# Optimization experiments

Measured on AMD Instinct MI355X. Metric: run time of the kernel, lower is better.

## Reference

```python
import jax, jax.numpy as jnp
import numpy as np

EPS_LN = 1e-5

def layer_norm(x, w, b):
    u = x.mean(-1, keepdims=True)
    s = jnp.mean((x - u) ** 2, -1, keepdims=True)
    return w * ((x - u) / jnp.sqrt(s + EPS_LN)) + b

def mlp(x, W, b, lw, lb):
    return jax.nn.relu(layer_norm(x @ W + b, lw, lb))

def mlp_gate(x, W, b, lw, lb):
    return jax.nn.sigmoid(layer_norm(x @ W + b, lw, lb))

def setup_inputs() -> dict:
    N, D = 768, 64
    key = jax.random.key(0)
    ks = jax.random.split(key, 12)
    inp = {
        'corr_index': jax.random.normal(ks[0], (N, N, 2), jnp.float32),
        'nei_index': jax.random.randint(ks[1], (N, N), 0, 2).astype(jnp.int64),
        'nei_num': jax.random.randint(ks[2], (N,), 0, N).astype(jnp.int64),
        'hidden_state': jax.random.normal(ks[3], (N, D), jnp.float32),
        'agent_v': jax.random.normal(ks[4], (N, 2), jnp.float32),
        # relativeLayer: MLP(3, D)
        'rel_w': jax.random.normal(ks[5], (3, D), jnp.float32) * (1.0 / np.sqrt(3)),
        'rel_b': jnp.zeros((D,), jnp.float32),
        'rel_lw': jnp.ones((D,), jnp.float32),
        'rel_lb': jnp.zeros((D,), jnp.float32),
        # ngate: MLP_gate(3D, D)
        'ng_w': jax.random.normal(ks[6], (3 * D, D), jnp.float32) * (1.0 / np.sqrt(3 * D)),
        'ng_b': jnp.zeros((D,), jnp.float32),
        'ng_lw': jnp.ones((D,), jnp.float32),
        'ng_lb': jnp.zeros((D,), jnp.float32),
        # WAr: MLP(3D, 1) -- LayerNorm(1) is identity in the source
        'war_w': jax.random.normal(ks[7], (3 * D, 1), jnp.float32) * (1.0 / np.sqrt(3 * D)),
        'war_b': jnp.zeros((1,), jnp.float32),
        # weight: MLP(D, D)
        'wt_w': jax.random.normal(ks[8], (D, D), jnp.float32) * (1.0 / np.sqrt(D)),
        'wt_b': jnp.zeros((D,), jnp.float32),
        'wt_lw': jnp.ones((D,), jnp.float32),
        'wt_lb': jnp.zeros((D,), jnp.float32),
    }
    return inp

def reference(corr_index, nei_index, nei_num, hidden_state, agent_v,
              rel_w, rel_b, rel_lw, rel_lb,
              ng_w, ng_b, ng_lw, ng_lb,
              war_w, war_b,
              wt_w, wt_b, wt_lw, wt_lb):
    N, D = hidden_state.shape
    # pair layout: row i*N+j  (i = receiver row of the NxN grid, j = column)
    agent_vt = jnp.tile(agent_v, (N, 1))                     # [N*N, 2], row i*N+j -> agent_v[j]
    corr_t = corr_index.reshape(N * N, 2)
    dot = agent_vt[:, 0] * corr_t[:, 0] + agent_vt[:, 1] * corr_t[:, 1]
    judge = jnp.sum(agent_vt ** 2, -1)
    angle = dot / (jnp.sqrt(judge * jnp.sum(corr_t ** 2, -1)) + 1e-10)
    angle = jnp.where(judge == 0, -1.0, angle)
    corr3 = jnp.concatenate([corr_t, angle[:, None]], -1)    # [N*N, 3]

    r_t = mlp(corr3, rel_w, rel_b, rel_lw, rel_lb)           # [N*N, D]
    nei_inputs = jnp.tile(hidden_state, (N, 1))              # row i*N+j -> h[j]
    hi_t = jnp.repeat(hidden_state, N, axis=0)               # row i*N+j -> h[i]
    tmp = jnp.concatenate([r_t, hi_t, nei_inputs], 1)        # [N*N, 3D]

    mask = (nei_index.reshape(N * N) > 0)
    nGate = mlp_gate(tmp, ng_w, ng_b, ng_lw, ng_lb)          # [N*N, D]
    tt = jax.nn.relu(tmp @ war_w + war_b).reshape(-1)        # LayerNorm(1) == identity

    Pos = jnp.where(mask, tt, 0.0).reshape(N, N)
    Pos = jnp.where(Pos == 0, -10000.0, Pos)
    Pos = jax.nn.softmax(Pos, axis=1)
    Pos_t = Pos.reshape(-1)

    H = jnp.where(mask[:, None], nei_inputs * nGate * Pos_t[:, None], 0.0)
    H_sum = mlp(H.reshape(N, N, D).sum(1), wt_w, wt_b, wt_lw, wt_lb)
    return hidden_state + H_sum
```

## Files before the change

kernel.cpp:

```cpp
#include <hip/hip_runtime.h>
#include <math.h>

#define NN 768
#define DD 64
#define WPB 4
#define HALVES 3
#define JW (NN / HALVES)
#define NSUB 4
#define RSTRIDE 34
#define PREBLKS 18
#define PSTRIDE 68
#define LOG2E 1.4426950408889634f

typedef _Float16 half8 __attribute__((ext_vector_type(8)));
typedef float    f32x4 __attribute__((ext_vector_type(4)));
typedef __fp16   p2f   __attribute__((ext_vector_type(2)));

union FragU { uint4 u4; unsigned int u[4]; half8 h; };
union PkU   { unsigned int u; p2f p; };

__device__ __forceinline__ unsigned int pk2(float a, float b) {
    PkU t; t.p = __builtin_amdgcn_cvt_pkrtz(a, b); return t.u;
}
__device__ __forceinline__ float lane_bcast(float v, int src) {
    return __int_as_float(__builtin_amdgcn_readlane(__float_as_int(v), src));
}
__device__ __forceinline__ float rfl(float v) {
    return __int_as_float(__builtin_amdgcn_readfirstlane(__float_as_int(v)));
}
__device__ __forceinline__ float fexp2(float x) {
    float r; asm("v_exp_f32 %0, %1" : "=v"(r) : "v"(x)); return r;
}
__device__ __forceinline__ float frcp(float x) {
    float r; asm("v_rcp_f32 %0, %1" : "=v"(r) : "v"(x)); return r;
}
__device__ __forceinline__ f32x4 mfma16(FragU a, FragU b, f32x4 c) {
    return __builtin_amdgcn_mfma_f32_16x16x32_f16(a.h, b.h, c, 0, 0, 0);
}

__global__ __launch_bounds__(256) void k_prepack(
    const float* __restrict__ hs, const float* __restrict__ ng_w,
    const float* __restrict__ ng_b, const float* __restrict__ war_w,
    const float* __restrict__ war_b,
    const float* __restrict__ rel_w, const float* __restrict__ rel_b,
    const float* __restrict__ rel_lw, const float* __restrict__ rel_lb,
    float* __restrict__ sbase, float* __restrict__ warb, float* __restrict__ war3,
    unsigned int* __restrict__ hf16,
    unsigned int* __restrict__ afragS, unsigned int* __restrict__ afragR,
    float* __restrict__ mom)
{
    const int t = threadIdx.x, blk = blockIdx.x;
    const int lane = t & 63, q = t >> 6, g = lane >> 4, c16 = lane & 15;

    if (blk >= PREBLKS) {
        const int row = (blk - PREBLKS) * 4 + q;
        const float hv = hs[row * DD + lane];
        float a2 = ng_b[lane];
        #pragma unroll 8
        for (int k = 0; k < DD; ++k)
            a2 = fmaf(lane_bcast(hv, k), ng_w[(DD + k) * DD + lane], a2);
        sbase[row * DD + lane] = a2;
        float t2 = hv * war_w[DD + lane];
        float t3 = hv * war_w[2 * DD + lane];
        #pragma unroll
        for (int o = 32; o; o >>= 1) { t2 += __shfl_xor(t2, o); t3 += __shfl_xor(t3, o); }
        if (lane == 0) {
            warb[row] = (t2 + war_b[0]) * LOG2E;
            war3[row] = t3 * LOG2E;
        }
        return;
    }

    for (int idx = blk * 256 + t; idx < NN * 32; idx += PREBLKS * 256) {
        const int row = idx >> 5, c = idx & 31;
        hf16[idx] = pk2(hs[row * DD + 2 * c], hs[row * DD + 2 * c + 1]);
    }

    if (blk < 16) {
        const int b = blk >> 2, c = blk & 3;
        const int dout = 16 * b + c16;
        const int k0 = 32 * c + g * 8 + 2 * q;
        const int r0 = (k0 < 64) ? k0 : (k0 + 64);
        afragS[(blk * 64 + lane) * 4 + q] =
            pk2(ng_w[r0 * DD + dout], ng_w[(r0 + 1) * DD + dout]);
    } else if (blk == 16) {
        const int b = q;
        const int d = 16 * b + c16;
        const float rlwd = rel_lw[d], rlbd = rel_lb[d];
        const float c0 = rel_w[d] * rlwd;
        const float c1 = rel_w[DD + d] * rlwd;
        const float c2 = rel_w[2 * DD + d] * rlwd;
        const float c3 = rel_b[d] * rlwd;
        PkU h01, h23, h45;
        h01.p = __builtin_amdgcn_cvt_pkrtz(c0, c1);
        h23.p = __builtin_amdgcn_cvt_pkrtz(c2, c3);
        h45.p = __builtin_amdgcn_cvt_pkrtz(rlwd, rlbd);
        const unsigned l01 = pk2(c0 - (float)h01.p[0], c1 - (float)h01.p[1]);
        const unsigned l23 = pk2(c2 - (float)h23.p[0], c3 - (float)h23.p[1]);
        const unsigned l45 = pk2(rlwd - (float)h45.p[0], rlbd - (float)h45.p[1]);
        const unsigned int base = (b * 64 + lane) * 4;
        unsigned v0, v1, v2;
        if (g == 0 || g == 1)      { v0 = h01.u; v1 = h23.u; v2 = h45.u; }
        else if (g == 2)           { v0 = l01;   v1 = l23;   v2 = l45;   }
        else                       { v0 = 0u;    v1 = 0u;    v2 = 0u;    }
        afragR[base + 0] = v0;
        afragR[base + 1] = v1;
        afragR[base + 2] = v2;
        afragR[base + 3] = 0u;
    } else {
        if (t < 64) {
            const float x0 = rel_w[t], x1 = rel_w[DD + t], x2 = rel_w[2 * DD + t];
            const float x3 = rel_b[t];
            float v[14] = {x0, x1, x2, x3,
                           x0 * x0, x1 * x1, x2 * x2, x3 * x3,
                           x0 * x1, x0 * x2, x0 * x3, x1 * x2, x1 * x3, x2 * x3};
            #pragma unroll
            for (int qq = 0; qq < 14; ++qq) {
                float s = v[qq];
                #pragma unroll
                for (int o = 32; o; o >>= 1) s += __shfl_xor(s, o);
                if (t == 0) mom[qq] = s * (1.f / 64.f);
            }
        }
    }
}

__global__ __launch_bounds__(64 * WPB) void k_main(
    const float* __restrict__ corr, const int* __restrict__ nei,
    const float* __restrict__ hs, const float* __restrict__ av,
    const float* __restrict__ ng_lw, const float* __restrict__ ng_lb,
    const float* __restrict__ war_w,
    const float* __restrict__ sbase, const float* __restrict__ warb,
    const float* __restrict__ war3,
    const unsigned int* __restrict__ afragS, const unsigned int* __restrict__ afragR,
    const unsigned int* __restrict__ hf16, const float* __restrict__ mom,
    float* __restrict__ part)
{
    const int h = blockIdx.x;
    const int i = blockIdx.y;
    const int tid = threadIdx.x;
    const int lane = tid & 63, wave = tid >> 6;
    const int g = lane >> 4, c16 = lane & 15;

    __shared__ uint4 sm_aS[16 * 64];
    __shared__ __align__(16) float sm_cst[4 * DD];
    __shared__ uint4 sm_b1h[WPB * 64];
    __shared__ uint4 sm_b1l[WPB * 64];
    __shared__ unsigned int smr[WPB * 16 * RSTRIDE];
    __shared__ float sm_red[WPB][DD];
    __shared__ float sm_m[WPB], sm_l[WPB];

    for (int f = tid; f < 16 * 64; f += 64 * WPB)
        sm_aS[f] = ((const uint4*)afragS)[f];
    {
        const int a = tid >> 6, d = tid & 63;
        float v;
        if (a == 0)      v = sbase[i * DD + d];
        else if (a == 1) v = war_w[d] * LOG2E;
        else if (a == 2) v = ng_lw[d] * LOG2E;
        else             v = ng_lb[d] * LOG2E;
        sm_cst[a * DD + d] = v;
    }

    FragU aR[4];
    #pragma unroll
    for (int b = 0; b < 4; ++b) aR[b].u4 = ((const uint4*)afragR)[b * 64 + lane];

    const float m0 = rfl(mom[0]), m1 = rfl(mom[1]), m2 = rfl(mom[2]), m3 = rfl(mom[3]);
    const float M00 = rfl(mom[4]), M11 = rfl(mom[5]), M22 = rfl(mom[6]), M33 = rfl(mom[7]);
    const float M01 = rfl(mom[8]), M02 = rfl(mom[9]), M03 = rfl(mom[10]);
    const float M12 = rfl(mom[11]), M13 = rfl(mom[12]), M23 = rfl(mom[13]);
    const float warbase = rfl(warb[i]);

    unsigned int* wrbase = smr + (wave * 16 + c16) * RSTRIDE;

    __syncthreads();

    const int jwbase = h * JW + wave * 64;
    {
        const int j = jwbase + lane;
        const float2 cc = ((const float2*)corr)[i * NN + j];
        const float2 vv = ((const float2*)av)[j];
        const float cx = cc.x, cy = cc.y;
        const float judge = vv.x * vv.x + vv.y * vv.y;
        const float dotv = fmaf(vv.x, cx, vv.y * cy);
        const float cn = cx * cx + cy * cy;
        float angle = __fdividef(dotv, sqrtf(judge * cn) + 1e-10f);
        if (judge == 0.f) angle = -1.f;

        const float u = fmaf(cx, m0, fmaf(cy, m1, fmaf(angle, m2, m3)));
        float e2 = M33;
        e2 = fmaf(cx * cx, M00, e2);
        e2 = fmaf(cy * cy, M11, e2);
        e2 = fmaf(angle * angle, M22, e2);
        e2 = fmaf(2.f * cx, fmaf(cy, M01, fmaf(angle, M02, M03)), e2);
        e2 = fmaf(2.f * cy, fmaf(angle, M12, M13), e2);
        e2 = fmaf(2.f * angle, M23, e2);
        const float vare = (e2 - u * u) + 1e-5f;
        const float inv = rsqrtf(vare);

        const float xc0 = cx * inv, xc1 = cy * inv, xc2 = angle * inv;
        const float xc3 = inv, xc4 = -u * inv;
        PkU s01, s23, s45;
        s01.p = __builtin_amdgcn_cvt_pkrtz(xc0, xc1);
        s23.p = __builtin_amdgcn_cvt_pkrtz(xc2, xc3);
        s45.p = __builtin_amdgcn_cvt_pkrtz(xc4, 1.f);
        const unsigned l0 = pk2(xc0 - (float)s01.p[0], xc1 - (float)s01.p[1]);
        const unsigned l1 = pk2(xc2 - (float)s23.p[0], xc3 - (float)s23.p[1]);
        const unsigned l2 = pk2(xc4 - (float)s45.p[0], 0.f);

        sm_b1h[wave * 64 + lane] = make_uint4(s01.u, s23.u, s45.u, 0u);
        sm_b1l[wave * 64 + lane] = make_uint4(l0, l1, l2, 0u);
    }

    float acc[16];
    #pragma unroll
    for (int x = 0; x < 16; ++x) acc[x] = 0.f;
    float mrun = -INFINITY, lrun = 0.f;

    unsigned zofs = 0;

    #pragma unroll 1
    for (int s = 0; s < NSUB; ++s) {
        asm volatile("" : "+v"(zofs));
        const uint4* aSp = sm_aS + zofs;
        const float* cst = sm_cst + zofs;

        const int jj = jwbase + 16 * s + c16;
        const int    nv = nei[i * NN + jj];
        const float  w3 = war3[jj];
        FragU bx2, bx3;
        bx2.u4 = *(const uint4*)(hf16 + jj * 32 + 4 * g);
        bx3.u4 = *(const uint4*)(hf16 + jj * 32 + 16 + 4 * g);

        FragU b1;
        {
            const int bi = wave * 64 + 16 * s + c16;
            const uint4 w = (g == 1) ? sm_b1l[bi] : sm_b1h[bi];
            b1.u[0] = (g == 3) ? 0u : w.x;
            b1.u[1] = (g == 3) ? 0u : w.y;
            b1.u[2] = (g == 3) ? 0u : w.z;
            b1.u[3] = 0u;
        }

        const f32x4 Z = {0.f, 0.f, 0.f, 0.f};
        float wd = 0.f;
        #pragma unroll
        for (int b = 0; b < 4; ++b) {
            const f32x4 P = mfma16(aR[b], b1, Z);
            const f32x4 wv = *(const f32x4*)(cst + 1 * DD + 16 * b + 4 * g);
            const float r0f = fmaxf(P[0], 0.f);
            const float r1f = fmaxf(P[1], 0.f);
            const float r2f = fmaxf(P[2], 0.f);
            const float r3f = fmaxf(P[3], 0.f);
            wd = fmaf(r0f, wv[0], wd);
            wd = fmaf(r1f, wv[1], wd);
            wd = fmaf(r2f, wv[2], wd);
            wd = fmaf(r3f, wv[3], wd);
            uint2 wvv;
            wvv.x = pk2(r0f, r1f);
            wvv.y = pk2(r2f, r3f);
            *(uint2*)(wrbase + 8 * b + 2 * g) = wvv;
        }

        FragU bx0, bx1;
        {
            const uint2 lo0 = *(const uint2*)(wrbase + 4 * g);
            const uint2 hi0 = *(const uint2*)(wrbase + 4 * g + 2);
            bx0.u[0] = lo0.x; bx0.u[1] = lo0.y; bx0.u[2] = hi0.x; bx0.u[3] = hi0.y;
            const uint2 lo1 = *(const uint2*)(wrbase + 16 + 4 * g);
            const uint2 hi1 = *(const uint2*)(wrbase + 16 + 4 * g + 2);
            bx1.u[0] = lo1.x; bx1.u[1] = lo1.y; bx1.u[2] = hi1.x; bx1.u[3] = hi1.y;
        }

        const f32x4 hv0 = *(const f32x4*)(hs + jj * DD +  0 + 4 * g);
        const f32x4 hv1 = *(const f32x4*)(hs + jj * DD + 16 + 4 * g);
        const f32x4 hv2 = *(const f32x4*)(hs + jj * DD + 32 + 4 * g);
        const f32x4 hv3 = *(const f32x4*)(hs + jj * DD + 48 + 4 * g);

        wd += __shfl_xor(wd, 16);
        wd += __shfl_xor(wd, 32);

        f32x4 S[4];
        #pragma unroll
        for (int b = 0; b < 4; ++b) {
            f32x4 cinit = *(const f32x4*)(cst + 0 * DD + 16 * b + 4 * g);
            FragU a2f, a3f, a0f, a1f;
            a2f.u4 = aSp[(b * 4 + 2) * 64 + lane];
            a3f.u4 = aSp[(b * 4 + 3) * 64 + lane];
            a0f.u4 = aSp[(b * 4 + 0) * 64 + lane];
            a1f.u4 = aSp[(b * 4 + 1) * 64 + lane];
            cinit = mfma16(a2f, bx2, cinit);
            cinit = mfma16(a3f, bx3, cinit);
            cinit = mfma16(a0f, bx0, cinit);
            cinit = mfma16(a1f, bx1, cinit);
            S[b] = cinit;
        }

        float s1 = 0.f, s2 = 0.f;
        #pragma unroll
        for (int x = 0; x < 16; ++x) {
            const float sv = S[x >> 2][x & 3];
            s1 += sv; s2 = fmaf(sv, sv, s2);
        }
        s1 += __shfl_xor(s1, 16); s1 += __shfl_xor(s1, 32);
        s2 += __shfl_xor(s2, 16); s2 += __shfl_xor(s2, 32);
        const float u2 = s1 * (1.f / 64.f);
        const float var2 = fmaf(s2, 1.f / 64.f, -u2 * u2);
        const float inv2 = rsqrtf(var2 + 1e-5f);

        const float tt = wd + w3 + warbase;
        const bool msk = nv > 0;
        const float p = (msk && tt > 0.f) ? tt : -10000.f;

        const float mn = fmaxf(mrun, p);
        const float alpha = fexp2(mrun - mn);
        const float e = fexp2(p - mn);
        const float eacc = msk ? e : 0.f;
        lrun = fmaf(lrun, alpha, e);
        mrun = mn;

        #pragma unroll
        for (int b = 0; b < 4; ++b) {
            const f32x4 hvb = (b == 0) ? hv0 : (b == 1) ? hv1 : (b == 2) ? hv2 : hv3;
            const f32x4 lw = *(const f32x4*)(cst + 2 * DD + 16 * b + 4 * g);
            const f32x4 lb = *(const f32x4*)(cst + 3 * DD + 16 * b + 4 * g);
            #pragma unroll
            for (int r = 0; r < 4; ++r) {
                const float ilw = inv2 * lw[r];
                const float blb = fmaf(-u2, ilw, lb[r]);
                const float ngv = fmaf(S[b][r], ilw, blb);
                const float gate = frcp(1.f + fexp2(-ngv));
                const float ehv = eacc * hvb[r];
                acc[b * 4 + r] = fmaf(acc[b * 4 + r], alpha, gate * ehv);
            }
        }
    }

    #pragma unroll
    for (int o = 1; o <= 8; o <<= 1) {
        const float mo  = __shfl_xor(mrun, o);
        const float lo_ = __shfl_xor(lrun, o);
        const float M   = fmaxf(mrun, mo);
        const float a1  = fexp2(mrun - M);
        const float a2  = fexp2(mo - M);
        lrun = lrun * a1 + lo_ * a2;
        #pragma unroll
        for (int x = 0; x < 16; ++x) {
            const float ao = __shfl_xor(acc[x], o);
            acc[x] = acc[x] * a1 + ao * a2;
        }
        mrun = M;
    }
    if (c16 == 0) {
        #pragma unroll
        for (int b = 0; b < 4; ++b)
            #pragma unroll
            for (int r = 0; r < 4; ++r)
                sm_red[wave][16 * b + g * 4 + r] = acc[b * 4 + r];
        if (lane == 0) { sm_m[wave] = mrun; sm_l[wave] = lrun; }
    }
    __syncthreads();

    if (tid < DD) {
        float M = sm_m[0];
        #pragma unroll
        for (int w = 1; w < WPB; ++w) M = fmaxf(M, sm_m[w]);
        float L = 0.f, A = 0.f;
        #pragma unroll
        for (int w = 0; w < WPB; ++w) {
            const float f = fexp2(sm_m[w] - M);
            L = fmaf(sm_l[w], f, L);
            A = fmaf(sm_red[w][tid], f, A);
        }
        float* p = part + (i * HALVES + h) * PSTRIDE;
        p[tid] = A;
        if (tid == 0) { p[64] = M; p[65] = L; }
    }
}

__global__ __launch_bounds__(64) void k_final(
    const float* __restrict__ hs, const float* __restrict__ part,
    const float* __restrict__ wt_w, const float* __restrict__ wt_b,
    const float* __restrict__ wt_lw, const float* __restrict__ wt_lb,
    float* __restrict__ out)
{
    const int i = blockIdx.x;
    const int tid = threadIdx.x;

    float ms[HALVES], ls[HALVES];
    float M = -INFINITY;
    #pragma unroll
    for (int hh = 0; hh < HALVES; ++hh) {
        const float* p = part + (i * HALVES + hh) * PSTRIDE;
        ms[hh] = p[64]; ls[hh] = p[65];
        M = fmaxf(M, ms[hh]);
    }
    float L = 0.f, A = 0.f;
    #pragma unroll
    for (int hh = 0; hh < HALVES; ++hh) {
        const float f = fexp2(ms[hh] - M);
        L = fmaf(ls[hh], f, L);
        A = fmaf(part[(i * HALVES + hh) * PSTRIDE + tid], f, A);
    }
    const float Hv = A / L;

    float v = wt_b[tid];
    #pragma unroll 8
    for (int k = 0; k < DD; ++k)
        v = fmaf(lane_bcast(Hv, k), wt_w[k * DD + tid], v);
    float t1 = v, t2 = v * v;
    #pragma unroll
    for (int o = 32; o; o >>= 1) { t1 += __shfl_xor(t1, o); t2 += __shfl_xor(t2, o); }
    const float uo = t1 * (1.f / 64.f);
    const float varo = fmaf(t2, 1.f / 64.f, -uo * uo);
    const float invo = rsqrtf(varo + 1e-5f);
    const float ro = fmaf((v - uo) * invo, wt_lw[tid], wt_lb[tid]);
    out[i * DD + tid] = hs[i * DD + tid] + fmaxf(ro, 0.f);
}

extern "C" void kernel_launch(void* const* d_in, const int* in_sizes, int n_in,
                              void* d_out, int out_size, void* d_ws, size_t ws_size,
                              hipStream_t stream) {
    const float* corr   = (const float*)d_in[0];
    const int*   nei    = (const int*)  d_in[1];
    const float* hs     = (const float*)d_in[3];
    const float* av     = (const float*)d_in[4];
    const float* rel_w  = (const float*)d_in[5];
    const float* rel_b  = (const float*)d_in[6];
    const float* rel_lw = (const float*)d_in[7];
    const float* rel_lb = (const float*)d_in[8];
    const float* ng_w   = (const float*)d_in[9];
    const float* ng_b   = (const float*)d_in[10];
    const float* ng_lw  = (const float*)d_in[11];
    const float* ng_lb  = (const float*)d_in[12];
    const float* war_w  = (const float*)d_in[13];
    const float* war_b  = (const float*)d_in[14];
    const float* wt_w   = (const float*)d_in[15];
    const float* wt_b   = (const float*)d_in[16];
    const float* wt_lw  = (const float*)d_in[17];
    const float* wt_lb  = (const float*)d_in[18];
    float* out = (float*)d_out;

    float* ws    = (float*)d_ws;
    float* sbase = ws;
    float* warb  = sbase + NN * DD;
    float* war3  = warb + NN;
    float* mom   = war3 + NN;
    unsigned int* hf16   = (unsigned int*)(mom + 16);
    unsigned int* afragS = hf16 + NN * 32;
    unsigned int* afragR = afragS + 16 * 64 * 4;
    float* part  = (float*)(afragR + 4 * 64 * 4);

    k_prepack<<<PREBLKS + NN / 4, 256, 0, stream>>>(
        hs, ng_w, ng_b, war_w, war_b, rel_w, rel_b, rel_lw, rel_lb,
        sbase, warb, war3, hf16, afragS, afragR, mom);
    k_main<<<dim3(HALVES, NN), 64 * WPB, 0, stream>>>(
        corr, nei, hs, av, ng_lw, ng_lb, war_w, sbase, warb, war3,
        afragS, afragR, hf16, mom, part);
    k_final<<<NN, 64, 0, stream>>>(
        hs, part, wt_w, wt_b, wt_lw, wt_lb, out);
}
```

Before: 137.4 us.

## Software-pipeline subtile loads and relative-MLP MFMA one iteration ahead

Moves the per-subtile global loads (neighbour mask, war3, fp16 and fp32 hidden rows) and the relative-position MFMA plus its LDS staging into a lambda. That lambda runs for subtile s+1 while subtile s does its gate MFMAs and softmax accumulation, hiding load and MFMA latency. The wd and LayerNorm sum reductions are also split into independent partial chains to shorten dependency chains. In exchange, register pressure rises from the double-buffered fragments, and the final iteration does a redundant phase for the same subtile.

```diff
diff --git a/kernel.cpp b/kernel.cpp
--- a/kernel.cpp
+++ b/kernel.cpp
@@ -213,29 +213,20 @@
         sm_b1l[wave * 64 + lane] = make_uint4(l0, l1, l2, 0u);
     }
 
-    float acc[16];
-    #pragma unroll
-    for (int x = 0; x < 16; ++x) acc[x] = 0.f;
-    float mrun = -INFINITY, lrun = 0.f;
-
-    unsigned zofs = 0;
-
-    #pragma unroll 1
-    for (int s = 0; s < NSUB; ++s) {
-        asm volatile("" : "+v"(zofs));
-        const uint4* aSp = sm_aS + zofs;
-        const float* cst = sm_cst + zofs;
-
-        const int jj = jwbase + 16 * s + c16;
-        const int    nv = nei[i * NN + jj];
-        const float  w3 = war3[jj];
-        FragU bx2, bx3;
-        bx2.u4 = *(const uint4*)(hf16 + jj * 32 + 4 * g);
-        bx3.u4 = *(const uint4*)(hf16 + jj * 32 + 16 + 4 * g);
+    auto phaseA = [&](int tt, const float* cst,
+                      int& NV, float& W3, FragU& BX2, FragU& BX3,
+                      FragU& BX0, FragU& BX1,
+                      f32x4& HV0, f32x4& HV1, f32x4& HV2, f32x4& HV3,
+                      float& WD) {
+        const int jj = jwbase + 16 * tt + c16;
+        NV = nei[i * NN + jj];
+        W3 = war3[jj];
+        BX2.u4 = *(const uint4*)(hf16 + jj * 32 + 4 * g);
+        BX3.u4 = *(const uint4*)(hf16 + jj * 32 + 16 + 4 * g);
 
         FragU b1;
         {
-            const int bi = wave * 64 + 16 * s + c16;
+            const int bi = wave * 64 + 16 * tt + c16;
             const uint4 w = (g == 1) ? sm_b1l[bi] : sm_b1h[bi];
             b1.u[0] = (g == 3) ? 0u : w.x;
             b1.u[1] = (g == 3) ? 0u : w.y;
@@ -244,7 +235,7 @@
         }
 
         const f32x4 Z = {0.f, 0.f, 0.f, 0.f};
-        float wd = 0.f;
+        float wdp[4];
         #pragma unroll
         for (int b = 0; b < 4; ++b) {
             const f32x4 P = mfma16(aR[b], b1, Z);
@@ -253,31 +244,60 @@
             const float r1f = fmaxf(P[1], 0.f);
             const float r2f = fmaxf(P[2], 0.f);
             const float r3f = fmaxf(P[3], 0.f);
-            wd = fmaf(r0f, wv[0], wd);
-            wd = fmaf(r1f, wv[1], wd);
-            wd = fmaf(r2f, wv[2], wd);
-            wd = fmaf(r3f, wv[3], wd);
+            float wp = r0f * wv[0];
+            wp = fmaf(r1f, wv[1], wp);
+            wp = fmaf(r2f, wv[2], wp);
+            wp = fmaf(r3f, wv[3], wp);
+            wdp[b] = wp;
             uint2 wvv;
             wvv.x = pk2(r0f, r1f);
             wvv.y = pk2(r2f, r3f);
             *(uint2*)(wrbase + 8 * b + 2 * g) = wvv;
         }
-
-        FragU bx0, bx1;
+        WD = (wdp[0] + wdp[1]) + (wdp[2] + wdp[3]);
+
         {
             const uint2 lo0 = *(const uint2*)(wrbase + 4 * g);
             const uint2 hi0 = *(const uint2*)(wrbase + 4 * g + 2);
-            bx0.u[0] = lo0.x; bx0.u[1] = lo0.y; bx0.u[2] = hi0.x; bx0.u[3] = hi0.y;
+            BX0.u[0] = lo0.x; BX0.u[1] = lo0.y; BX0.u[2] = hi0.x; BX0.u[3] = hi0.y;
             const uint2 lo1 = *(const uint2*)(wrbase + 16 + 4 * g);
             const uint2 hi1 = *(const uint2*)(wrbase + 16 + 4 * g + 2);
-            bx1.u[0] = lo1.x; bx1.u[1] = lo1.y; bx1.u[2] = hi1.x; bx1.u[3] = hi1.y;
-        }
-
-        const f32x4 hv0 = *(const f32x4*)(hs + jj * DD +  0 + 4 * g);
-        const f32x4 hv1 = *(const f32x4*)(hs + jj * DD + 16 + 4 * g);
-        const f32x4 hv2 = *(const f32x4*)(hs + jj * DD + 32 + 4 * g);
-        const f32x4 hv3 = *(const f32x4*)(hs + jj * DD + 48 + 4 * g);
-
+            BX1.u[0] = lo1.x; BX1.u[1] = lo1.y; BX1.u[2] = hi1.x; BX1.u[3] = hi1.y;
+        }
+
+        HV0 = *(const f32x4*)(hs + jj * DD +  0 + 4 * g);
+        HV1 = *(const f32x4*)(hs + jj * DD + 16 + 4 * g);
+        HV2 = *(const f32x4*)(hs + jj * DD + 32 + 4 * g);
+        HV3 = *(const f32x4*)(hs + jj * DD + 48 + 4 * g);
+    };
+
+    float acc[16];
+    #pragma unroll
+    for (int x = 0; x < 16; ++x) acc[x] = 0.f;
+    float mrun = -INFINITY, lrun = 0.f;
+
+    int   nv_c;  float w3_c, wd_c;
+    FragU bx2_c, bx3_c, bx0_c, bx1_c;
+    f32x4 hv0_c, hv1_c, hv2_c, hv3_c;
+    phaseA(0, sm_cst, nv_c, w3_c, bx2_c, bx3_c, bx0_c, bx1_c,
+           hv0_c, hv1_c, hv2_c, hv3_c, wd_c);
+
+    unsigned zofs = 0;
+
+    #pragma unroll 1
+    for (int s = 0; s < NSUB; ++s) {
+        asm volatile("" : "+v"(zofs));
+        const uint4* aSp = sm_aS + zofs;
+        const float* cst = sm_cst + zofs;
+
+        const int tn = (s + 1 < NSUB) ? s + 1 : s;
+        int   nv_n;  float w3_n, wd_n;
+        FragU bx2_n, bx3_n, bx0_n, bx1_n;
+        f32x4 hv0_n, hv1_n, hv2_n, hv3_n;
+        phaseA(tn, cst, nv_n, w3_n, bx2_n, bx3_n, bx0_n, bx1_n,
+               hv0_n, hv1_n, hv2_n, hv3_n, wd_n);
+
+        float wd = wd_c;
         wd += __shfl_xor(wd, 16);
         wd += __shfl_xor(wd, 32);
 
@@ -290,27 +310,33 @@
             a3f.u4 = aSp[(b * 4 + 3) * 64 + lane];
             a0f.u4 = aSp[(b * 4 + 0) * 64 + lane];
             a1f.u4 = aSp[(b * 4 + 1) * 64 + lane];
-            cinit = mfma16(a2f, bx2, cinit);
-            cinit = mfma16(a3f, bx3, cinit);
-            cinit = mfma16(a0f, bx0, cinit);
-            cinit = mfma16(a1f, bx1, cinit);
+            cinit = mfma16(a2f, bx2_c, cinit);
+            cinit = mfma16(a3f, bx3_c, cinit);
+            cinit = mfma16(a0f, bx0_c, cinit);
+            cinit = mfma16(a1f, bx1_c, cinit);
             S[b] = cinit;
         }
 
-        float s1 = 0.f, s2 = 0.f;
-        #pragma unroll
-        for (int x = 0; x < 16; ++x) {
+        float s1a = 0.f, s1b = 0.f, s2a = 0.f, s2b = 0.f;
+        #pragma unroll
+        for (int x = 0; x < 8; ++x) {
             const float sv = S[x >> 2][x & 3];
-            s1 += sv; s2 = fmaf(sv, sv, s2);
-        }
+            s1a += sv; s2a = fmaf(sv, sv, s2a);
+        }
+        #pragma unroll
+        for (int x = 8; x < 16; ++x) {
+            const float sv = S[x >> 2][x & 3];
+            s1b += sv; s2b = fmaf(sv, sv, s2b);
+        }
+        float s1 = s1a + s1b, s2 = s2a + s2b;
         s1 += __shfl_xor(s1, 16); s1 += __shfl_xor(s1, 32);
         s2 += __shfl_xor(s2, 16); s2 += __shfl_xor(s2, 32);
         const float u2 = s1 * (1.f / 64.f);
         const float var2 = fmaf(s2, 1.f / 64.f, -u2 * u2);
         const float inv2 = rsqrtf(var2 + 1e-5f);
 
-        const float tt = wd + w3 + warbase;
-        const bool msk = nv > 0;
+        const float tt = wd + w3_c + warbase;
+        const bool msk = nv_c > 0;
         const float p = (msk && tt > 0.f) ? tt : -10000.f;
 
         const float mn = fmaxf(mrun, p);
@@ -322,7 +348,8 @@
 
         #pragma unroll
         for (int b = 0; b < 4; ++b) {
-            const f32x4 hvb = (b == 0) ? hv0 : (b == 1) ? hv1 : (b == 2) ? hv2 : hv3;
+            const f32x4 hvb = (b == 0) ? hv0_c : (b == 1) ? hv1_c
+                           : (b == 2) ? hv2_c : hv3_c;
             const f32x4 lw = *(const f32x4*)(cst + 2 * DD + 16 * b + 4 * g);
             const f32x4 lb = *(const f32x4*)(cst + 3 * DD + 16 * b + 4 * g);
             #pragma unroll
@@ -335,6 +362,10 @@
                 acc[b * 4 + r] = fmaf(acc[b * 4 + r], alpha, gate * ehv);
             }
         }
+
+        nv_c = nv_n; w3_c = w3_n; wd_c = wd_n;
+        bx2_c = bx2_n; bx3_c = bx3_n; bx0_c = bx0_n; bx1_c = bx1_n;
+        hv0_c = hv0_n; hv1_c = hv1_n; hv2_c = hv2_n; hv3_c = hv3_n;
     }
 
     #pragma unroll
```

Measured after the change: 143.9 us. 1.05x slower.
